# Performance work log

Measured on AMD Instinct MI355X. Metric: run time of the kernel, lower is better.

Reference implementation:

```python
import jax, jax.numpy as jnp
import numpy as np

B, MSG, H, D, N = 64, 64, 512, 512, 2048


def setup_inputs() -> dict:
    key = jax.random.key(0)
    ks = jax.random.split(key, 20)
    s = 0.02
    return {
        "message": jax.random.normal(ks[0], (B, MSG), jnp.float32),
        "state": jax.random.normal(ks[1], (B, H), jnp.float32),
        "image": jax.random.normal(ks[2], (B, H), jnp.float32),
        "class_descriptors": jax.random.normal(ks[3], (N, D), jnp.float32),
        # GRUCell params (torch layout: gates ordered r, z, n)
        "w_ih": jax.random.normal(ks[4], (3 * H, MSG), jnp.float32) * s,
        "w_hh": jax.random.normal(ks[5], (3 * H, H), jnp.float32) * s,
        "b_ih": jax.random.normal(ks[6], (3 * H,), jnp.float32) * s,
        "b_hh": jax.random.normal(ks[7], (3 * H,), jnp.float32) * s,
        "w_stop": jax.random.normal(ks[8], (1, H), jnp.float32) * s,
        "b_stop": jax.random.normal(ks[9], (1,), jnp.float32) * s,
        "w_y1": jax.random.normal(ks[10], (H, H + D), jnp.float32) * s,
        "b_y1": jax.random.normal(ks[11], (H,), jnp.float32) * s,
        "w_y2": jax.random.normal(ks[12], (1, H), jnp.float32) * s,
        "b_y2": jax.random.normal(ks[13], (1,), jnp.float32) * s,
        "w_state": jax.random.normal(ks[14], (H, H), jnp.float32) * s,
        "b_state": jax.random.normal(ks[15], (H,), jnp.float32) * s,
        "w_desc": jax.random.normal(ks[16], (H, D), jnp.float32) * s,  # no bias
        "w_msg": jax.random.normal(ks[17], (MSG, H), jnp.float32) * s,
        "b_msg": jax.random.normal(ks[18], (MSG,), jnp.float32) * s,
    }


def _gru_cell(x, h, w_ih, w_hh, b_ih, b_hh):
    gi = x @ w_ih.T + b_ih  # [B, 3H]
    gh = h @ w_hh.T + b_hh
    i_r, i_z, i_n = jnp.split(gi, 3, axis=1)
    h_r, h_z, h_n = jnp.split(gh, 3, axis=1)
    r = jax.nn.sigmoid(i_r + h_r)
    z = jax.nn.sigmoid(i_z + h_z)
    n = jnp.tanh(i_n + r * h_n)
    return (1.0 - z) * n + z * h


def reference(message, state, image, class_descriptors,
              w_ih, w_hh, b_ih, b_hh, w_stop, b_stop,
              w_y1, b_y1, w_y2, b_y2, w_state, b_state,
              w_desc, w_msg, b_msg):
    b, h = state.shape
    n, d = class_descriptors.shape

    new_state = _gru_cell(message, state, w_ih, w_hh, b_ih, b_hh)  # [B, H]
    stop_dist = jax.nn.sigmoid(new_state @ w_stop.T + b_stop)  # [B, 1]
    stop_bit = jax.lax.stop_gradient(jnp.round(stop_dist))  # eval-mode path

    # build_state_descriptor_pairs (faithful to torch view semantics,
    # including the (B, H, N) -> (B*N, H) interleaved reshape of pair_left)
    pair_left = jnp.broadcast_to(new_state[:, :, None], (b, h, n)).reshape(b * n, h)
    pair_right = jnp.broadcast_to(class_descriptors[None], (b, n, d)).reshape(b * n, d)
    pairs = jnp.concatenate([pair_left, pair_right], axis=1)  # [B*N, H+D]

    y = jnp.clip(pairs @ w_y1.T + b_y1, 0.0, None)  # relu, [B*N, H]
    y = (y @ w_y2.T + b_y2).reshape(b, -1)  # [B, N]
    y_scores = jax.lax.stop_gradient(jax.nn.softmax(y, axis=1))

    # reweight_descriptors: softmax-weighted sum over descriptors
    descriptor_influence = jnp.einsum('bn,nd->bd', y_scores, class_descriptors)

    message_state = jnp.tanh(new_state @ w_state.T + b_state
                             + descriptor_influence @ w_desc.T)
    message_dist = jax.nn.sigmoid(message_state @ w_msg.T + b_msg)  # [B, MSG]
    outp_msg = jax.lax.stop_gradient(jnp.round(message_dist))

    return stop_bit, stop_dist, outp_msg, message_dist, y
```

## Files before the change

### kernel.cpp

```cpp
#include <hip/hip_runtime.h>
#include <hip/hip_bf16.h>


__device__ __forceinline__ float sigm(float x) { return 1.0f / (1.0f + expf(-x)); }

__global__ __launch_bounds__(64) void gru_kernel(
    const float* __restrict__ msg, const float* __restrict__ st,
    const float* __restrict__ w_ih, const float* __restrict__ w_hh,
    const float* __restrict__ b_ih, const float* __restrict__ b_hh,
    float* __restrict__ ns, float* __restrict__ nsT) {
  const int h = blockIdx.x;
  const int bi = threadIdx.x;
  __shared__ __align__(16) float sIr[64], sIz[64], sIn[64];
  __shared__ __align__(16) float sHr[512], sHz[512], sHn[512];
  sIr[bi] = w_ih[h * 64 + bi];
  sIz[bi] = w_ih[(h + 512) * 64 + bi];
  sIn[bi] = w_ih[(h + 1024) * 64 + bi];
  {
    float4* r4 = (float4*)sHr; const float4* gr = (const float4*)(w_hh + h * 512);
    float4* z4 = (float4*)sHz; const float4* gz = (const float4*)(w_hh + (h + 512) * 512);
    float4* n4 = (float4*)sHn; const float4* gn = (const float4*)(w_hh + (h + 1024) * 512);
    for (int i = bi; i < 128; i += 64) { r4[i] = gr[i]; z4[i] = gz[i]; n4[i] = gn[i]; }
  }
  __syncthreads();
  float ir = b_ih[h], iz = b_ih[h + 512], inn = b_ih[h + 1024];
  float hr = b_hh[h], hz = b_hh[h + 512], hn = b_hh[h + 1024];
  const float* mrow = msg + bi * 64;
  #pragma unroll 4
  for (int m = 0; m < 64; m += 4) {
    float4 x = *(const float4*)&mrow[m];
    float4 wr = *(const float4*)&sIr[m];
    float4 wz = *(const float4*)&sIz[m];
    float4 wn = *(const float4*)&sIn[m];
    ir = fmaf(x.x, wr.x, ir); ir = fmaf(x.y, wr.y, ir); ir = fmaf(x.z, wr.z, ir); ir = fmaf(x.w, wr.w, ir);
    iz = fmaf(x.x, wz.x, iz); iz = fmaf(x.y, wz.y, iz); iz = fmaf(x.z, wz.z, iz); iz = fmaf(x.w, wz.w, iz);
    inn = fmaf(x.x, wn.x, inn); inn = fmaf(x.y, wn.y, inn); inn = fmaf(x.z, wn.z, inn); inn = fmaf(x.w, wn.w, inn);
  }
  const float* srow = st + bi * 512;
  float hprev = srow[h];
  #pragma unroll 4
  for (int k = 0; k < 512; k += 4) {
    float4 x = *(const float4*)&srow[k];
    float4 wr = *(const float4*)&sHr[k];
    float4 wz = *(const float4*)&sHz[k];
    float4 wn = *(const float4*)&sHn[k];
    hr = fmaf(x.x, wr.x, hr); hr = fmaf(x.y, wr.y, hr); hr = fmaf(x.z, wr.z, hr); hr = fmaf(x.w, wr.w, hr);
    hz = fmaf(x.x, wz.x, hz); hz = fmaf(x.y, wz.y, hz); hz = fmaf(x.z, wz.z, hz); hz = fmaf(x.w, wz.w, hz);
    hn = fmaf(x.x, wn.x, hn); hn = fmaf(x.y, wn.y, hn); hn = fmaf(x.z, wn.z, hn); hn = fmaf(x.w, wn.w, hn);
  }
  float r = sigm(ir + hr);
  float z = sigm(iz + hz);
  float n = tanhf(inn + r * hn);
  float v = (1.0f - z) * n + z * hprev;
  ns[bi * 512 + h] = v;
  nsT[h * 64 + bi] = v;
}

__global__ __launch_bounds__(512) void stop_kernel(
    const float* __restrict__ ns, const float* __restrict__ w_stop,
    const float* __restrict__ b_stop, float* __restrict__ out_bit,
    float* __restrict__ out_dist) {
  __shared__ __align__(16) float sw[512];
  __shared__ float sp[512];
  const int t = threadIdx.x;
  sw[t] = w_stop[t];
  __syncthreads();
  const int bi = t >> 3, kg = t & 7;
  const float* row = ns + bi * 512 + kg * 64;
  const float* wrow = sw + kg * 64;
  float acc = 0.0f;
  #pragma unroll 4
  for (int k = 0; k < 64; k += 4) {
    float4 r = *(const float4*)&row[k];
    float4 w = *(const float4*)&wrow[k];
    acc = fmaf(r.x, w.x, acc); acc = fmaf(r.y, w.y, acc);
    acc = fmaf(r.z, w.z, acc); acc = fmaf(r.w, w.w, acc);
  }
  sp[t] = acc;
  __syncthreads();
  if (t < 64) {
    float s = b_stop[0];
    #pragma unroll
    for (int g = 0; g < 8; ++g) s += sp[t * 8 + g];
    float sd = sigm(s);
    out_dist[t] = sd;
    out_bit[t] = rintf(sd);
  }
}

__global__ __launch_bounds__(64) void ws1_kernel(const float* __restrict__ w_y1,
                                                 float* __restrict__ ws1) {
  const int j = blockIdx.x;
  const int t = threadIdx.x;
  const float* row = w_y1 + j * 1024;
  float acc = 0.0f;
  #pragma unroll
  for (int c = t; c < 512; c += 64) acc += row[c];
  #pragma unroll
  for (int s = 32; s > 0; s >>= 1) acc += __shfl_down(acc, s, 64);
  if (t == 0) ws1[j] = acc;
}

#define GBK 16
__global__ __launch_bounds__(256) void g_kernel(
    const float* __restrict__ desc, const float* __restrict__ w_y1,
    const float* __restrict__ b_y1, float* __restrict__ G) {
  __shared__ __align__(16) float As[GBK][64];
  __shared__ __align__(16) float Bs[GBK][64];
  const int rr0 = blockIdx.x * 64;
  const int j0 = blockIdx.y * 64;
  const int tid = threadIdx.x;
  const int tm = (tid >> 4) * 4;
  const int tn = (tid & 15) * 4;
  const int lm = tid >> 2;
  const int lkq = (tid & 3) * 4;
  float acc[4][4] = {};
  for (int k0 = 0; k0 < 512; k0 += GBK) {
    float4 av = *(const float4*)&desc[(rr0 + lm) * 512 + k0 + lkq];
    float4 bv = *(const float4*)&w_y1[(j0 + lm) * 1024 + 512 + k0 + lkq];
    __syncthreads();
    As[lkq + 0][lm] = av.x; As[lkq + 1][lm] = av.y;
    As[lkq + 2][lm] = av.z; As[lkq + 3][lm] = av.w;
    Bs[lkq + 0][lm] = bv.x; Bs[lkq + 1][lm] = bv.y;
    Bs[lkq + 2][lm] = bv.z; Bs[lkq + 3][lm] = bv.w;
    __syncthreads();
    #pragma unroll
    for (int k = 0; k < GBK; ++k) {
      float4 a = *(const float4*)&As[k][tm];
      float4 b = *(const float4*)&Bs[k][tn];
      acc[0][0] = fmaf(a.x, b.x, acc[0][0]); acc[0][1] = fmaf(a.x, b.y, acc[0][1]);
      acc[0][2] = fmaf(a.x, b.z, acc[0][2]); acc[0][3] = fmaf(a.x, b.w, acc[0][3]);
      acc[1][0] = fmaf(a.y, b.x, acc[1][0]); acc[1][1] = fmaf(a.y, b.y, acc[1][1]);
      acc[1][2] = fmaf(a.y, b.z, acc[1][2]); acc[1][3] = fmaf(a.y, b.w, acc[1][3]);
      acc[2][0] = fmaf(a.z, b.x, acc[2][0]); acc[2][1] = fmaf(a.z, b.y, acc[2][1]);
      acc[2][2] = fmaf(a.z, b.z, acc[2][2]); acc[2][3] = fmaf(a.z, b.w, acc[2][3]);
      acc[3][0] = fmaf(a.w, b.x, acc[3][0]); acc[3][1] = fmaf(a.w, b.y, acc[3][1]);
      acc[3][2] = fmaf(a.w, b.z, acc[3][2]); acc[3][3] = fmaf(a.w, b.w, acc[3][3]);
    }
  }
  #pragma unroll
  for (int j = 0; j < 4; ++j) {
    float by = b_y1[j0 + tn + j];
    #pragma unroll
    for (int i = 0; i < 4; ++i) {
      G[(rr0 + tm + i) * 512 + j0 + tn + j] = acc[i][j] + by;
    }
  }
}

__global__ __launch_bounds__(64) void y_kernel(
    const float* __restrict__ nsT, const float* __restrict__ ws1,
    const float* __restrict__ G, const float* __restrict__ w_y2,
    const float* __restrict__ b_y2, float* __restrict__ yf) {
  const int rr = blockIdx.x;
  const int bi = threadIdx.x;
  __shared__ __align__(16) float sG[512], sW1[512], sW2[512];
  {
    float4* g4 = (float4*)sG;  const float4* gg = (const float4*)(G + rr * 512);
    float4* a4 = (float4*)sW1; const float4* ga = (const float4*)ws1;
    float4* b4 = (float4*)sW2; const float4* gb = (const float4*)w_y2;
    for (int i = bi; i < 128; i += 64) { g4[i] = gg[i]; a4[i] = ga[i]; b4[i] = gb[i]; }
  }
  __syncthreads();
  const float v = nsT[(rr >> 2) * 64 + bi];
  float acc = 0.0f;
  #pragma unroll 4
  for (int j = 0; j < 512; j += 4) {
    float4 g = *(const float4*)&sG[j];
    float4 w1 = *(const float4*)&sW1[j];
    float4 w2 = *(const float4*)&sW2[j];
    acc = fmaf(w2.x, fmaxf(fmaf(v, w1.x, g.x), 0.0f), acc);
    acc = fmaf(w2.y, fmaxf(fmaf(v, w1.y, g.y), 0.0f), acc);
    acc = fmaf(w2.z, fmaxf(fmaf(v, w1.z, g.z), 0.0f), acc);
    acc = fmaf(w2.w, fmaxf(fmaf(v, w1.w, g.w), 0.0f), acc);
  }
  yf[bi * 2048 + rr] = acc + b_y2[0];
}

__global__ __launch_bounds__(256) void softmax_kernel(
    const float* __restrict__ yf, float* __restrict__ scores,
    float* __restrict__ out_y) {
  const int bi = blockIdx.x;
  const int t = threadIdx.x;
  __shared__ float sy[2048];
  __shared__ float red[256];
  float lmax = -3.0e38f;
  for (int i = t; i < 2048; i += 256) {
    float v = yf[bi * 2048 + i];
    sy[i] = v;
    out_y[bi * 2048 + i] = v;
    lmax = fmaxf(lmax, v);
  }
  red[t] = lmax;
  __syncthreads();
  for (int s = 128; s > 0; s >>= 1) {
    if (t < s) red[t] = fmaxf(red[t], red[t + s]);
    __syncthreads();
  }
  const float mx = red[0];
  __syncthreads();
  float lsum = 0.0f;
  for (int i = t; i < 2048; i += 256) {
    float e = expf(sy[i] - mx);
    sy[i] = e;
    lsum += e;
  }
  red[t] = lsum;
  __syncthreads();
  for (int s = 128; s > 0; s >>= 1) {
    if (t < s) red[t] += red[t + s];
    __syncthreads();
  }
  const float inv = 1.0f / red[0];
  for (int i = t; i < 2048; i += 256) scores[bi * 2048 + i] = sy[i] * inv;
}

__global__ __launch_bounds__(256) void di_part_kernel(
    const float* __restrict__ scores, const float* __restrict__ desc,
    float* __restrict__ dp) {
  __shared__ __align__(16) float sS[64][64];
  __shared__ __align__(16) float sD[64][64];
  const int d0 = blockIdx.x * 64;
  const int n0 = blockIdx.y * 64;
  const int tid = threadIdx.x;
  {
    const int bi = tid >> 2;
    #pragma unroll
    for (int i = 0; i < 4; ++i) {
      const int kq = (tid & 3) * 4 + i * 16;
      float4 av = *(const float4*)&scores[bi * 2048 + n0 + kq];
      sS[kq + 0][bi] = av.x; sS[kq + 1][bi] = av.y;
      sS[kq + 2][bi] = av.z; sS[kq + 3][bi] = av.w;
    }
  }
  {
    #pragma unroll
    for (int i = 0; i < 4; ++i) {
      const int nn = (tid >> 4) + i * 16;
      const int dq = (tid & 15) * 4;
      *(float4*)&sD[nn][dq] = *(const float4*)&desc[(n0 + nn) * 512 + d0 + dq];
    }
  }
  __syncthreads();
  const int bi0 = (tid >> 4) * 4;
  const int dd0 = (tid & 15) * 4;
  float acc[4][4] = {};
  #pragma unroll 8
  for (int nn = 0; nn < 64; ++nn) {
    float4 a = *(const float4*)&sS[nn][bi0];
    float4 b = *(const float4*)&sD[nn][dd0];
    acc[0][0] = fmaf(a.x, b.x, acc[0][0]); acc[0][1] = fmaf(a.x, b.y, acc[0][1]);
    acc[0][2] = fmaf(a.x, b.z, acc[0][2]); acc[0][3] = fmaf(a.x, b.w, acc[0][3]);
    acc[1][0] = fmaf(a.y, b.x, acc[1][0]); acc[1][1] = fmaf(a.y, b.y, acc[1][1]);
    acc[1][2] = fmaf(a.y, b.z, acc[1][2]); acc[1][3] = fmaf(a.y, b.w, acc[1][3]);
    acc[2][0] = fmaf(a.z, b.x, acc[2][0]); acc[2][1] = fmaf(a.z, b.y, acc[2][1]);
    acc[2][2] = fmaf(a.z, b.z, acc[2][2]); acc[2][3] = fmaf(a.z, b.w, acc[2][3]);
    acc[3][0] = fmaf(a.w, b.x, acc[3][0]); acc[3][1] = fmaf(a.w, b.y, acc[3][1]);
    acc[3][2] = fmaf(a.w, b.z, acc[3][2]); acc[3][3] = fmaf(a.w, b.w, acc[3][3]);
  }
  float* base = dp + blockIdx.y * 32768;
  #pragma unroll
  for (int i = 0; i < 4; ++i)
    #pragma unroll
    for (int j = 0; j < 4; ++j)
      base[(bi0 + i) * 512 + d0 + dd0 + j] = acc[i][j];
}

__global__ __launch_bounds__(512) void di_reduce_kernel(
    const float* __restrict__ dp, float* __restrict__ di) {
  const int idx = blockIdx.x * 512 + threadIdx.x;
  float acc = 0.0f;
  #pragma unroll 8
  for (int c = 0; c < 32; ++c) acc += dp[c * 32768 + idx];
  di[idx] = acc;
}

__global__ __launch_bounds__(64) void ms_kernel(
    const float* __restrict__ ns, const float* __restrict__ di,
    const float* __restrict__ w_state, const float* __restrict__ b_state,
    const float* __restrict__ w_desc, float* __restrict__ ms) {
  const int hj = blockIdx.x;
  const int bi = threadIdx.x;
  __shared__ __align__(16) float sWs[512], sWd[512];
  {
    float4* a4 = (float4*)sWs; const float4* ga = (const float4*)(w_state + hj * 512);
    float4* b4 = (float4*)sWd; const float4* gb = (const float4*)(w_desc + hj * 512);
    for (int i = bi; i < 128; i += 64) { a4[i] = ga[i]; b4[i] = gb[i]; }
  }
  __syncthreads();
  float acc = b_state[hj];
  const float* nr = ns + bi * 512;
  const float* dr = di + bi * 512;
  #pragma unroll 4
  for (int k = 0; k < 512; k += 4) {
    float4 a = *(const float4*)&nr[k];
    float4 w = *(const float4*)&sWs[k];
    float4 b = *(const float4*)&dr[k];
    float4 u = *(const float4*)&sWd[k];
    acc = fmaf(a.x, w.x, acc); acc = fmaf(a.y, w.y, acc);
    acc = fmaf(a.z, w.z, acc); acc = fmaf(a.w, w.w, acc);
    acc = fmaf(b.x, u.x, acc); acc = fmaf(b.y, u.y, acc);
    acc = fmaf(b.z, u.z, acc); acc = fmaf(b.w, u.w, acc);
  }
  ms[bi * 512 + hj] = tanhf(acc);
}

__global__ __launch_bounds__(64) void msg_kernel(
    const float* __restrict__ ms, const float* __restrict__ w_msg,
    const float* __restrict__ b_msg, float* __restrict__ out_msg,
    float* __restrict__ out_msgdist) {
  const int m = blockIdx.x;
  const int bi = threadIdx.x;
  __shared__ __align__(16) float sW[512];
  {
    float4* a4 = (float4*)sW; const float4* ga = (const float4*)(w_msg + m * 512);
    for (int i = bi; i < 128; i += 64) a4[i] = ga[i];
  }
  __syncthreads();
  float acc = b_msg[m];
  const float* row = ms + bi * 512;
  #pragma unroll 4
  for (int k = 0; k < 512; k += 4) {
    float4 a = *(const float4*)&row[k];
    float4 w = *(const float4*)&sW[k];
    acc = fmaf(a.x, w.x, acc); acc = fmaf(a.y, w.y, acc);
    acc = fmaf(a.z, w.z, acc); acc = fmaf(a.w, w.w, acc);
  }
  float md = sigm(acc);
  out_msgdist[bi * 64 + m] = md;
  out_msg[bi * 64 + m] = rintf(md);
}

extern "C" void kernel_launch(void* const* d_in, const int* in_sizes, int n_in,
                              void* d_out, int out_size, void* d_ws, size_t ws_size,
                              hipStream_t stream) {
  (void)in_sizes; (void)n_in; (void)out_size; (void)ws_size;
  const float* message = (const float*)d_in[0];
  const float* state   = (const float*)d_in[1];
  const float* desc    = (const float*)d_in[3];
  const float* w_ih    = (const float*)d_in[4];
  const float* w_hh    = (const float*)d_in[5];
  const float* b_ih    = (const float*)d_in[6];
  const float* b_hh    = (const float*)d_in[7];
  const float* w_stop  = (const float*)d_in[8];
  const float* b_stop  = (const float*)d_in[9];
  const float* w_y1    = (const float*)d_in[10];
  const float* b_y1    = (const float*)d_in[11];
  const float* w_y2    = (const float*)d_in[12];
  const float* b_y2    = (const float*)d_in[13];
  const float* w_state = (const float*)d_in[14];
  const float* b_state = (const float*)d_in[15];
  const float* w_desc  = (const float*)d_in[16];
  const float* w_msg   = (const float*)d_in[17];
  const float* b_msg   = (const float*)d_in[18];

  float* out = (float*)d_out;
  float* out_stopbit  = out;
  float* out_stopdist = out + 64;
  float* out_msg      = out + 128;
  float* out_msgdist  = out + 4224;
  float* out_y        = out + 8320;

  char* ws = (char*)d_ws;
  float* ns     = (float*)(ws);
  float* ws1    = (float*)(ws + 131072);
  float* G      = (float*)(ws + 133120);
  float* yf     = (float*)(ws + 4327424);
  float* scores = (float*)(ws + 4851712);
  float* di     = (float*)(ws + 5376000);
  float* ms     = (float*)(ws + 5507072);
  float* nsT    = (float*)(ws + 5638144);

  gru_kernel<<<512, 64, 0, stream>>>(message, state, w_ih, w_hh, b_ih, b_hh, ns, nsT);
  stop_kernel<<<1, 512, 0, stream>>>(ns, w_stop, b_stop, out_stopbit, out_stopdist);
  ws1_kernel<<<512, 64, 0, stream>>>(w_y1, ws1);
  g_kernel<<<dim3(32, 8), 256, 0, stream>>>(desc, w_y1, b_y1, G);
  y_kernel<<<2048, 64, 0, stream>>>(nsT, ws1, G, w_y2, b_y2, yf);
  softmax_kernel<<<64, 256, 0, stream>>>(yf, scores, out_y);
  di_part_kernel<<<dim3(8, 32), 256, 0, stream>>>(scores, desc, G);
  di_reduce_kernel<<<64, 512, 0, stream>>>(G, di);
  ms_kernel<<<512, 64, 0, stream>>>(ns, di, w_state, b_state, w_desc, ms);
  msg_kernel<<<64, 64, 0, stream>>>(ms, w_msg, b_msg, out_msg, out_msgdist);
}
```

Baseline: 201.7 us.

## Fuse y computation into G GEMM epilogue, merge stop/ws1, widen GEMV blocks

The y_kernel is folded into the g_kernel epilogue. Each block evaluates relu(v*ws1+G)·w_y2 for all 64 batch rows and writes partial sums per j-tile, which softmax then adds up, so the G intermediate no longer round-trips through memory. The stop and ws1 kernels are merged into one launch. The GRU, ms and msg kernels move to 512 threads per block with split-K across 8 lanes, padded shared staging and shuffle reductions. The G GEMM also gains register prefetch of the next tile. The trade-offs are more partial-sum traffic into softmax and a serial 64-iteration epilogue per block.

```diff
diff --git a/kernel.cpp b/kernel.cpp
--- a/kernel.cpp
+++ b/kernel.cpp
@@ -4,109 +4,122 @@
 
 __device__ __forceinline__ float sigm(float x) { return 1.0f / (1.0f + expf(-x)); }
 
-__global__ __launch_bounds__(64) void gru_kernel(
+__device__ __forceinline__ void stage_pad68(float* dst, const float* src, int c) {
+  *(float4*)&dst[(c >> 4) * 68 + (c & 15) * 4] = *(const float4*)&src[c * 4];
+}
+
+__global__ __launch_bounds__(512) void gru_kernel(
     const float* __restrict__ msg, const float* __restrict__ st,
     const float* __restrict__ w_ih, const float* __restrict__ w_hh,
     const float* __restrict__ b_ih, const float* __restrict__ b_hh,
     float* __restrict__ ns, float* __restrict__ nsT) {
   const int h = blockIdx.x;
-  const int bi = threadIdx.x;
+  const int t = threadIdx.x;
+  __shared__ __align__(16) float sHr[544], sHz[544], sHn[544];
   __shared__ __align__(16) float sIr[64], sIz[64], sIn[64];
-  __shared__ __align__(16) float sHr[512], sHz[512], sHn[512];
-  sIr[bi] = w_ih[h * 64 + bi];
-  sIz[bi] = w_ih[(h + 512) * 64 + bi];
-  sIn[bi] = w_ih[(h + 1024) * 64 + bi];
-  {
-    float4* r4 = (float4*)sHr; const float4* gr = (const float4*)(w_hh + h * 512);
-    float4* z4 = (float4*)sHz; const float4* gz = (const float4*)(w_hh + (h + 512) * 512);
-    float4* n4 = (float4*)sHn; const float4* gn = (const float4*)(w_hh + (h + 1024) * 512);
-    for (int i = bi; i < 128; i += 64) { r4[i] = gr[i]; z4[i] = gz[i]; n4[i] = gn[i]; }
-  }
-  __syncthreads();
-  float ir = b_ih[h], iz = b_ih[h + 512], inn = b_ih[h + 1024];
-  float hr = b_hh[h], hz = b_hh[h + 512], hn = b_hh[h + 1024];
-  const float* mrow = msg + bi * 64;
-  #pragma unroll 4
-  for (int m = 0; m < 64; m += 4) {
-    float4 x = *(const float4*)&mrow[m];
-    float4 wr = *(const float4*)&sIr[m];
-    float4 wz = *(const float4*)&sIz[m];
-    float4 wn = *(const float4*)&sIn[m];
-    ir = fmaf(x.x, wr.x, ir); ir = fmaf(x.y, wr.y, ir); ir = fmaf(x.z, wr.z, ir); ir = fmaf(x.w, wr.w, ir);
-    iz = fmaf(x.x, wz.x, iz); iz = fmaf(x.y, wz.y, iz); iz = fmaf(x.z, wz.z, iz); iz = fmaf(x.w, wz.w, iz);
-    inn = fmaf(x.x, wn.x, inn); inn = fmaf(x.y, wn.y, inn); inn = fmaf(x.z, wn.z, inn); inn = fmaf(x.w, wn.w, inn);
-  }
-  const float* srow = st + bi * 512;
-  float hprev = srow[h];
-  #pragma unroll 4
-  for (int k = 0; k < 512; k += 4) {
-    float4 x = *(const float4*)&srow[k];
-    float4 wr = *(const float4*)&sHr[k];
-    float4 wz = *(const float4*)&sHz[k];
-    float4 wn = *(const float4*)&sHn[k];
-    hr = fmaf(x.x, wr.x, hr); hr = fmaf(x.y, wr.y, hr); hr = fmaf(x.z, wr.z, hr); hr = fmaf(x.w, wr.w, hr);
-    hz = fmaf(x.x, wz.x, hz); hz = fmaf(x.y, wz.y, hz); hz = fmaf(x.z, wz.z, hz); hz = fmaf(x.w, wz.w, hz);
-    hn = fmaf(x.x, wn.x, hn); hn = fmaf(x.y, wn.y, hn); hn = fmaf(x.z, wn.z, hn); hn = fmaf(x.w, wn.w, hn);
-  }
-  float r = sigm(ir + hr);
-  float z = sigm(iz + hz);
-  float n = tanhf(inn + r * hn);
-  float v = (1.0f - z) * n + z * hprev;
-  ns[bi * 512 + h] = v;
-  nsT[h * 64 + bi] = v;
-}
-
-__global__ __launch_bounds__(512) void stop_kernel(
+  if (t < 128)      stage_pad68(sHr, w_hh + h * 512, t);
+  else if (t < 256) stage_pad68(sHz, w_hh + (h + 512) * 512, t - 128);
+  else if (t < 384) stage_pad68(sHn, w_hh + (h + 1024) * 512, t - 256);
+  else if (t < 400) ((float4*)sIr)[t - 384] = ((const float4*)(w_ih + h * 64))[t - 384];
+  else if (t < 416) ((float4*)sIz)[t - 400] = ((const float4*)(w_ih + (h + 512) * 64))[t - 400];
+  else if (t < 432) ((float4*)sIn)[t - 416] = ((const float4*)(w_ih + (h + 1024) * 64))[t - 416];
+  __syncthreads();
+  const int bi = t >> 3, kg = t & 7;
+  float pr = 0.f, pz = 0.f, pin = 0.f, phn = 0.f;
+  {
+    const float* mrow = msg + bi * 64 + kg * 8;
+    const float* ir = &sIr[kg * 8];
+    const float* iz = &sIz[kg * 8];
+    const float* in_ = &sIn[kg * 8];
+    #pragma unroll
+    for (int i = 0; i < 2; ++i) {
+      float4 x = *(const float4*)&mrow[i * 4];
+      float4 wr = *(const float4*)&ir[i * 4];
+      float4 wz = *(const float4*)&iz[i * 4];
+      float4 wn = *(const float4*)&in_[i * 4];
+      pr = fmaf(x.x, wr.x, pr); pr = fmaf(x.y, wr.y, pr); pr = fmaf(x.z, wr.z, pr); pr = fmaf(x.w, wr.w, pr);
+      pz = fmaf(x.x, wz.x, pz); pz = fmaf(x.y, wz.y, pz); pz = fmaf(x.z, wz.z, pz); pz = fmaf(x.w, wz.w, pz);
+      pin = fmaf(x.x, wn.x, pin); pin = fmaf(x.y, wn.y, pin); pin = fmaf(x.z, wn.z, pin); pin = fmaf(x.w, wn.w, pin);
+    }
+  }
+  {
+    const float* srow = st + bi * 512 + kg * 64;
+    const float* hr = &sHr[kg * 68];
+    const float* hz = &sHz[kg * 68];
+    const float* hn = &sHn[kg * 68];
+    #pragma unroll
+    for (int i = 0; i < 16; ++i) {
+      float4 x = *(const float4*)&srow[i * 4];
+      float4 wr = *(const float4*)&hr[i * 4];
+      float4 wz = *(const float4*)&hz[i * 4];
+      float4 wn = *(const float4*)&hn[i * 4];
+      pr = fmaf(x.x, wr.x, pr); pr = fmaf(x.y, wr.y, pr); pr = fmaf(x.z, wr.z, pr); pr = fmaf(x.w, wr.w, pr);
+      pz = fmaf(x.x, wz.x, pz); pz = fmaf(x.y, wz.y, pz); pz = fmaf(x.z, wz.z, pz); pz = fmaf(x.w, wz.w, pz);
+      phn = fmaf(x.x, wn.x, phn); phn = fmaf(x.y, wn.y, phn); phn = fmaf(x.z, wn.z, phn); phn = fmaf(x.w, wn.w, phn);
+    }
+  }
+  pr += __shfl_xor(pr, 1, 8); pr += __shfl_xor(pr, 2, 8); pr += __shfl_xor(pr, 4, 8);
+  pz += __shfl_xor(pz, 1, 8); pz += __shfl_xor(pz, 2, 8); pz += __shfl_xor(pz, 4, 8);
+  pin += __shfl_xor(pin, 1, 8); pin += __shfl_xor(pin, 2, 8); pin += __shfl_xor(pin, 4, 8);
+  phn += __shfl_xor(phn, 1, 8); phn += __shfl_xor(phn, 2, 8); phn += __shfl_xor(phn, 4, 8);
+  if ((t & 7) == 0) {
+    float r = sigm(pr + b_ih[h] + b_hh[h]);
+    float z = sigm(pz + b_ih[h + 512] + b_hh[h + 512]);
+    float n = tanhf(pin + b_ih[h + 1024] + r * (phn + b_hh[h + 1024]));
+    float hp = st[bi * 512 + h];
+    float v = (1.0f - z) * n + z * hp;
+    ns[bi * 512 + h] = v;
+    nsT[h * 64 + bi] = v;
+  }
+}
+
+__global__ __launch_bounds__(512) void stopws1_kernel(
+    const float* __restrict__ w_y1, float* __restrict__ ws1,
     const float* __restrict__ ns, const float* __restrict__ w_stop,
     const float* __restrict__ b_stop, float* __restrict__ out_bit,
     float* __restrict__ out_dist) {
-  __shared__ __align__(16) float sw[512];
-  __shared__ float sp[512];
   const int t = threadIdx.x;
-  sw[t] = w_stop[t];
-  __syncthreads();
-  const int bi = t >> 3, kg = t & 7;
-  const float* row = ns + bi * 512 + kg * 64;
-  const float* wrow = sw + kg * 64;
-  float acc = 0.0f;
-  #pragma unroll 4
-  for (int k = 0; k < 64; k += 4) {
-    float4 r = *(const float4*)&row[k];
-    float4 w = *(const float4*)&wrow[k];
-    acc = fmaf(r.x, w.x, acc); acc = fmaf(r.y, w.y, acc);
-    acc = fmaf(r.z, w.z, acc); acc = fmaf(r.w, w.w, acc);
-  }
-  sp[t] = acc;
-  __syncthreads();
-  if (t < 64) {
-    float s = b_stop[0];
-    #pragma unroll
-    for (int g = 0; g < 8; ++g) s += sp[t * 8 + g];
-    float sd = sigm(s);
-    out_dist[t] = sd;
-    out_bit[t] = rintf(sd);
-  }
-}
-
-__global__ __launch_bounds__(64) void ws1_kernel(const float* __restrict__ w_y1,
-                                                 float* __restrict__ ws1) {
-  const int j = blockIdx.x;
-  const int t = threadIdx.x;
-  const float* row = w_y1 + j * 1024;
-  float acc = 0.0f;
-  #pragma unroll
-  for (int c = t; c < 512; c += 64) acc += row[c];
-  #pragma unroll
-  for (int s = 32; s > 0; s >>= 1) acc += __shfl_down(acc, s, 64);
-  if (t == 0) ws1[j] = acc;
+  if (blockIdx.x < 64) {
+    const int j = blockIdx.x * 8 + (t >> 6);
+    const int lane = t & 63;
+    const float* row = w_y1 + j * 1024 + lane * 8;
+    float4 a = *(const float4*)&row[0];
+    float4 b = *(const float4*)&row[4];
+    float acc = a.x + a.y + a.z + a.w + b.x + b.y + b.z + b.w;
+    #pragma unroll
+    for (int m = 1; m < 64; m <<= 1) acc += __shfl_xor(acc, m, 64);
+    if (lane == 0) ws1[j] = acc;
+  } else {
+    const int bi = t >> 3, kg = t & 7;
+    const float* row = ns + bi * 512 + kg * 64;
+    const float* wrow = w_stop + kg * 64;
+    float acc = 0.f;
+    #pragma unroll
+    for (int i = 0; i < 16; ++i) {
+      float4 r = *(const float4*)&row[i * 4];
+      float4 w = *(const float4*)&wrow[i * 4];
+      acc = fmaf(r.x, w.x, acc); acc = fmaf(r.y, w.y, acc);
+      acc = fmaf(r.z, w.z, acc); acc = fmaf(r.w, w.w, acc);
+    }
+    acc += __shfl_xor(acc, 1, 8); acc += __shfl_xor(acc, 2, 8); acc += __shfl_xor(acc, 4, 8);
+    if ((t & 7) == 0) {
+      float sd = sigm(acc + b_stop[0]);
+      out_dist[bi] = sd;
+      out_bit[bi] = rintf(sd);
+    }
+  }
 }
 
 #define GBK 16
 __global__ __launch_bounds__(256) void g_kernel(
     const float* __restrict__ desc, const float* __restrict__ w_y1,
-    const float* __restrict__ b_y1, float* __restrict__ G) {
+    const float* __restrict__ b_y1, const float* __restrict__ nsT,
+    const float* __restrict__ ws1, const float* __restrict__ w_y2,
+    float* __restrict__ yp) {
   __shared__ __align__(16) float As[GBK][64];
   __shared__ __align__(16) float Bs[GBK][64];
+  __shared__ __align__(16) float sV[16][66];
+  __shared__ __align__(16) float sW1[64], sW2[64];
   const int rr0 = blockIdx.x * 64;
   const int j0 = blockIdx.y * 64;
   const int tid = threadIdx.x;
@@ -114,16 +127,27 @@
   const int tn = (tid & 15) * 4;
   const int lm = tid >> 2;
   const int lkq = (tid & 3) * 4;
+  {
+    const int q = tid >> 4, pos = (tid & 15) * 4;
+    *(float4*)&sV[q][pos] = *(const float4*)&nsT[((rr0 >> 2) + q) * 64 + pos];
+  }
+  if (tid < 64) { sW1[tid] = ws1[j0 + tid]; sW2[tid] = w_y2[j0 + tid]; }
   float acc[4][4] = {};
+  const float* aptr = desc + (rr0 + lm) * 512 + lkq;
+  const float* bptr = w_y1 + (j0 + lm) * 1024 + 512 + lkq;
+  float4 av = *(const float4*)aptr;
+  float4 bv = *(const float4*)bptr;
   for (int k0 = 0; k0 < 512; k0 += GBK) {
-    float4 av = *(const float4*)&desc[(rr0 + lm) * 512 + k0 + lkq];
-    float4 bv = *(const float4*)&w_y1[(j0 + lm) * 1024 + 512 + k0 + lkq];
     __syncthreads();
     As[lkq + 0][lm] = av.x; As[lkq + 1][lm] = av.y;
     As[lkq + 2][lm] = av.z; As[lkq + 3][lm] = av.w;
     Bs[lkq + 0][lm] = bv.x; Bs[lkq + 1][lm] = bv.y;
     Bs[lkq + 2][lm] = bv.z; Bs[lkq + 3][lm] = bv.w;
     __syncthreads();
+    if (k0 + GBK < 512) {
+      av = *(const float4*)(aptr + k0 + GBK);
+      bv = *(const float4*)(bptr + k0 + GBK);
+    }
     #pragma unroll
     for (int k = 0; k < GBK; ++k) {
       float4 a = *(const float4*)&As[k][tm];
@@ -138,55 +162,56 @@
       acc[3][2] = fmaf(a.w, b.z, acc[3][2]); acc[3][3] = fmaf(a.w, b.w, acc[3][3]);
     }
   }
-  #pragma unroll
-  for (int j = 0; j < 4; ++j) {
-    float by = b_y1[j0 + tn + j];
+  {
+    float4 by = *(const float4*)&b_y1[j0 + tn];
     #pragma unroll
     for (int i = 0; i < 4; ++i) {
-      G[(rr0 + tm + i) * 512 + j0 + tn + j] = acc[i][j] + by;
-    }
-  }
-}
-
-__global__ __launch_bounds__(64) void y_kernel(
-    const float* __restrict__ nsT, const float* __restrict__ ws1,
-    const float* __restrict__ G, const float* __restrict__ w_y2,
-    const float* __restrict__ b_y2, float* __restrict__ yf) {
-  const int rr = blockIdx.x;
-  const int bi = threadIdx.x;
-  __shared__ __align__(16) float sG[512], sW1[512], sW2[512];
-  {
-    float4* g4 = (float4*)sG;  const float4* gg = (const float4*)(G + rr * 512);
-    float4* a4 = (float4*)sW1; const float4* ga = (const float4*)ws1;
-    float4* b4 = (float4*)sW2; const float4* gb = (const float4*)w_y2;
-    for (int i = bi; i < 128; i += 64) { g4[i] = gg[i]; a4[i] = ga[i]; b4[i] = gb[i]; }
-  }
-  __syncthreads();
-  const float v = nsT[(rr >> 2) * 64 + bi];
-  float acc = 0.0f;
-  #pragma unroll 4
-  for (int j = 0; j < 512; j += 4) {
-    float4 g = *(const float4*)&sG[j];
-    float4 w1 = *(const float4*)&sW1[j];
-    float4 w2 = *(const float4*)&sW2[j];
-    acc = fmaf(w2.x, fmaxf(fmaf(v, w1.x, g.x), 0.0f), acc);
-    acc = fmaf(w2.y, fmaxf(fmaf(v, w1.y, g.y), 0.0f), acc);
-    acc = fmaf(w2.z, fmaxf(fmaf(v, w1.z, g.z), 0.0f), acc);
-    acc = fmaf(w2.w, fmaxf(fmaf(v, w1.w, g.w), 0.0f), acc);
-  }
-  yf[bi * 2048 + rr] = acc + b_y2[0];
+      acc[i][0] += by.x; acc[i][1] += by.y; acc[i][2] += by.z; acc[i][3] += by.w;
+    }
+  }
+  const float4 w1 = *(const float4*)&sW1[tn];
+  const float4 w2 = *(const float4*)&sW2[tn];
+  const int vrow = tid >> 4;
+  float* ypb = yp + blockIdx.y * 131072 + rr0 + tm;
+  for (int bi = 0; bi < 64; ++bi) {
+    const float v = sV[vrow][bi];
+    float p0 = fmaf(w2.x, fmaxf(fmaf(v, w1.x, acc[0][0]), 0.f),
+               fmaf(w2.y, fmaxf(fmaf(v, w1.y, acc[0][1]), 0.f),
+               fmaf(w2.z, fmaxf(fmaf(v, w1.z, acc[0][2]), 0.f),
+                    w2.w * fmaxf(fmaf(v, w1.w, acc[0][3]), 0.f))));
+    float p1 = fmaf(w2.x, fmaxf(fmaf(v, w1.x, acc[1][0]), 0.f),
+               fmaf(w2.y, fmaxf(fmaf(v, w1.y, acc[1][1]), 0.f),
+               fmaf(w2.z, fmaxf(fmaf(v, w1.z, acc[1][2]), 0.f),
+                    w2.w * fmaxf(fmaf(v, w1.w, acc[1][3]), 0.f))));
+    float p2 = fmaf(w2.x, fmaxf(fmaf(v, w1.x, acc[2][0]), 0.f),
+               fmaf(w2.y, fmaxf(fmaf(v, w1.y, acc[2][1]), 0.f),
+               fmaf(w2.z, fmaxf(fmaf(v, w1.z, acc[2][2]), 0.f),
+                    w2.w * fmaxf(fmaf(v, w1.w, acc[2][3]), 0.f))));
+    float p3 = fmaf(w2.x, fmaxf(fmaf(v, w1.x, acc[3][0]), 0.f),
+               fmaf(w2.y, fmaxf(fmaf(v, w1.y, acc[3][1]), 0.f),
+               fmaf(w2.z, fmaxf(fmaf(v, w1.z, acc[3][2]), 0.f),
+                    w2.w * fmaxf(fmaf(v, w1.w, acc[3][3]), 0.f))));
+    p0 += __shfl_xor(p0, 1, 16); p0 += __shfl_xor(p0, 2, 16); p0 += __shfl_xor(p0, 4, 16); p0 += __shfl_xor(p0, 8, 16);
+    p1 += __shfl_xor(p1, 1, 16); p1 += __shfl_xor(p1, 2, 16); p1 += __shfl_xor(p1, 4, 16); p1 += __shfl_xor(p1, 8, 16);
+    p2 += __shfl_xor(p2, 1, 16); p2 += __shfl_xor(p2, 2, 16); p2 += __shfl_xor(p2, 4, 16); p2 += __shfl_xor(p2, 8, 16);
+    p3 += __shfl_xor(p3, 1, 16); p3 += __shfl_xor(p3, 2, 16); p3 += __shfl_xor(p3, 4, 16); p3 += __shfl_xor(p3, 8, 16);
+    if ((tid & 15) == 0) *(float4*)&ypb[bi * 2048] = make_float4(p0, p1, p2, p3);
+  }
 }
 
 __global__ __launch_bounds__(256) void softmax_kernel(
-    const float* __restrict__ yf, float* __restrict__ scores,
-    float* __restrict__ out_y) {
+    const float* __restrict__ yp, const float* __restrict__ b_y2,
+    float* __restrict__ scores, float* __restrict__ out_y) {
   const int bi = blockIdx.x;
   const int t = threadIdx.x;
   __shared__ float sy[2048];
   __shared__ float red[256];
+  const float b = b_y2[0];
   float lmax = -3.0e38f;
   for (int i = t; i < 2048; i += 256) {
-    float v = yf[bi * 2048 + i];
+    const float* p = yp + bi * 2048 + i;
+    float v = b + p[0] + p[131072] + p[262144] + p[393216]
+                + p[524288] + p[655360] + p[786432] + p[917504];
     sy[i] = v;
     out_y[bi * 2048 + i] = v;
     lmax = fmaxf(lmax, v);
@@ -275,60 +300,63 @@
   di[idx] = acc;
 }
 
-__global__ __launch_bounds__(64) void ms_kernel(
+__global__ __launch_bounds__(512) void ms_kernel(
     const float* __restrict__ ns, const float* __restrict__ di,
     const float* __restrict__ w_state, const float* __restrict__ b_state,
     const float* __restrict__ w_desc, float* __restrict__ ms) {
   const int hj = blockIdx.x;
-  const int bi = threadIdx.x;
-  __shared__ __align__(16) float sWs[512], sWd[512];
-  {
-    float4* a4 = (float4*)sWs; const float4* ga = (const float4*)(w_state + hj * 512);
-    float4* b4 = (float4*)sWd; const float4* gb = (const float4*)(w_desc + hj * 512);
-    for (int i = bi; i < 128; i += 64) { a4[i] = ga[i]; b4[i] = gb[i]; }
-  }
-  __syncthreads();
-  float acc = b_state[hj];
-  const float* nr = ns + bi * 512;
-  const float* dr = di + bi * 512;
-  #pragma unroll 4
-  for (int k = 0; k < 512; k += 4) {
-    float4 a = *(const float4*)&nr[k];
-    float4 w = *(const float4*)&sWs[k];
-    float4 b = *(const float4*)&dr[k];
-    float4 u = *(const float4*)&sWd[k];
+  const int t = threadIdx.x;
+  __shared__ __align__(16) float sWs[544], sWd[544];
+  if (t < 128)      stage_pad68(sWs, w_state + hj * 512, t);
+  else if (t < 256) stage_pad68(sWd, w_desc + hj * 512, t - 128);
+  __syncthreads();
+  const int bi = t >> 3, kg = t & 7;
+  const float* nr = ns + bi * 512 + kg * 64;
+  const float* dr = di + bi * 512 + kg * 64;
+  const float* wsp = &sWs[kg * 68];
+  const float* wdp = &sWd[kg * 68];
+  float acc = 0.f;
+  #pragma unroll
+  for (int i = 0; i < 16; ++i) {
+    float4 a = *(const float4*)&nr[i * 4];
+    float4 w = *(const float4*)&wsp[i * 4];
+    float4 b = *(const float4*)&dr[i * 4];
+    float4 u = *(const float4*)&wdp[i * 4];
     acc = fmaf(a.x, w.x, acc); acc = fmaf(a.y, w.y, acc);
     acc = fmaf(a.z, w.z, acc); acc = fmaf(a.w, w.w, acc);
     acc = fmaf(b.x, u.x, acc); acc = fmaf(b.y, u.y, acc);
     acc = fmaf(b.z, u.z, acc); acc = fmaf(b.w, u.w, acc);
   }
-  ms[bi * 512 + hj] = tanhf(acc);
-}
-
-__global__ __launch_bounds__(64) void msg_kernel(
+  acc += __shfl_xor(acc, 1, 8); acc += __shfl_xor(acc, 2, 8); acc += __shfl_xor(acc, 4, 8);
+  if ((t & 7) == 0) ms[bi * 512 + hj] = tanhf(acc + b_state[hj]);
+}
+
+__global__ __launch_bounds__(512) void msg_kernel(
     const float* __restrict__ ms, const float* __restrict__ w_msg,
     const float* __restrict__ b_msg, float* __restrict__ out_msg,
     float* __restrict__ out_msgdist) {
   const int m = blockIdx.x;
-  const int bi = threadIdx.x;
-  __shared__ __align__(16) float sW[512];
-  {
-    float4* a4 = (float4*)sW; const float4* ga = (const float4*)(w_msg + m * 512);
-    for (int i = bi; i < 128; i += 64) a4[i] = ga[i];
-  }
-  __syncthreads();
-  float acc = b_msg[m];
-  const float* row = ms + bi * 512;
-  #pragma unroll 4
-  for (int k = 0; k < 512; k += 4) {
-    float4 a = *(const float4*)&row[k];
-    float4 w = *(const float4*)&sW[k];
+  const int t = threadIdx.x;
+  __shared__ __align__(16) float sW[544];
+  if (t < 128) stage_pad68(sW, w_msg + m * 512, t);
+  __syncthreads();
+  const int bi = t >> 3, kg = t & 7;
+  const float* row = ms + bi * 512 + kg * 64;
+  const float* wp = &sW[kg * 68];
+  float acc = 0.f;
+  #pragma unroll
+  for (int i = 0; i < 16; ++i) {
+    float4 a = *(const float4*)&row[i * 4];
+    float4 w = *(const float4*)&wp[i * 4];
     acc = fmaf(a.x, w.x, acc); acc = fmaf(a.y, w.y, acc);
     acc = fmaf(a.z, w.z, acc); acc = fmaf(a.w, w.w, acc);
   }
-  float md = sigm(acc);
-  out_msgdist[bi * 64 + m] = md;
-  out_msg[bi * 64 + m] = rintf(md);
+  acc += __shfl_xor(acc, 1, 8); acc += __shfl_xor(acc, 2, 8); acc += __shfl_xor(acc, 4, 8);
+  if ((t & 7) == 0) {
+    float md = sigm(acc + b_msg[m]);
+    out_msgdist[bi * 64 + m] = md;
+    out_msg[bi * 64 + m] = rintf(md);
+  }
 }
 
 extern "C" void kernel_launch(void* const* d_in, const int* in_sizes, int n_in,
@@ -363,22 +391,19 @@
 
   char* ws = (char*)d_ws;
   float* ns     = (float*)(ws);
-  float* ws1    = (float*)(ws + 131072);
-  float* G      = (float*)(ws + 133120);
-  float* yf     = (float*)(ws + 4327424);
-  float* scores = (float*)(ws + 4851712);
-  float* di     = (float*)(ws + 5376000);
-  float* ms     = (float*)(ws + 5507072);
-  float* nsT    = (float*)(ws + 5638144);
-
-  gru_kernel<<<512, 64, 0, stream>>>(message, state, w_ih, w_hh, b_ih, b_hh, ns, nsT);
-  stop_kernel<<<1, 512, 0, stream>>>(ns, w_stop, b_stop, out_stopbit, out_stopdist);
-  ws1_kernel<<<512, 64, 0, stream>>>(w_y1, ws1);
-  g_kernel<<<dim3(32, 8), 256, 0, stream>>>(desc, w_y1, b_y1, G);
-  y_kernel<<<2048, 64, 0, stream>>>(nsT, ws1, G, w_y2, b_y2, yf);
-  softmax_kernel<<<64, 256, 0, stream>>>(yf, scores, out_y);
-  di_part_kernel<<<dim3(8, 32), 256, 0, stream>>>(scores, desc, G);
-  di_reduce_kernel<<<64, 512, 0, stream>>>(G, di);
-  ms_kernel<<<512, 64, 0, stream>>>(ns, di, w_state, b_state, w_desc, ms);
-  msg_kernel<<<64, 64, 0, stream>>>(ms, w_msg, b_msg, out_msg, out_msgdist);
-}
+  float* nsT    = (float*)(ws + 131072);
+  float* ws1    = (float*)(ws + 262144);
+  float* yp     = (float*)(ws + 270336);
+  float* scores = (float*)(ws + 4988928);
+  float* di     = (float*)(ws + 5513216);
+  float* ms     = (float*)(ws + 5644288);
+
+  gru_kernel<<<512, 512, 0, stream>>>(message, state, w_ih, w_hh, b_ih, b_hh, ns, nsT);
+  stopws1_kernel<<<65, 512, 0, stream>>>(w_y1, ws1, ns, w_stop, b_stop, out_stopbit, out_stopdist);
+  g_kernel<<<dim3(32, 8), 256, 0, stream>>>(desc, w_y1, b_y1, nsT, ws1, w_y2, yp);
+  softmax_kernel<<<64, 256, 0, stream>>>(yp, b_y2, scores, out_y);
+  di_part_kernel<<<dim3(8, 32), 256, 0, stream>>>(scores, desc, yp);
+  di_reduce_kernel<<<64, 512, 0, stream>>>(yp, di);
+  ms_kernel<<<512, 512, 0, stream>>>(ns, di, w_state, b_state, w_desc, ms);
+  msg_kernel<<<64, 512, 0, stream>>>(ms, w_msg, b_msg, out_msg, out_msgdist);
+}
```

After: 213.8 us. 1.06x slower.
